# Kernel optimization log

Measured on AMD Instinct MI355X. Metric: run time of the kernel, lower is better.

## Reference

```python
import jax, jax.numpy as jnp
import numpy as np

L, N, H = 32768, 256, 256


def _binop(ei, ej):
    a_i, bu_i = ei
    a_j, bu_j = ej
    return (a_j * a_i, a_j * bu_i + bu_j)


def setup_inputs() -> dict:
    key = jax.random.key(0)
    ks = jax.random.split(key, 9)
    # Param values follow init_lru_parameters statistics for numerical sanity.
    u1 = jax.random.uniform(ks[0], (N,), minval=1e-3, maxval=1.0)
    u2 = jax.random.uniform(ks[1], (N,), minval=1e-3, maxval=1.0)
    nu_log = jnp.log(-0.5 * jnp.log(u1))
    theta_log = jnp.log(6.28 * u2)
    B_re = jax.random.normal(ks[2], (N, H)) / np.sqrt(2.0 * H)
    B_im = jax.random.normal(ks[3], (N, H)) / np.sqrt(2.0 * H)
    C_re = jax.random.normal(ks[4], (H, N)) / np.sqrt(1.0 * N)
    C_im = jax.random.normal(ks[5], (H, N)) / np.sqrt(1.0 * N)
    D = jax.random.normal(ks[6], (H,))
    diag_lambda = jnp.exp(-jnp.exp(nu_log) + 1j * jnp.exp(theta_log))
    gamma_log = jnp.log(jnp.sqrt(1.0 - jnp.abs(diag_lambda) ** 2))
    x = jax.random.normal(ks[7], (L, H), dtype=jnp.float32)
    f32 = lambda a: a.astype(jnp.float32)
    return {"x": x, "nu_log": f32(nu_log), "theta_log": f32(theta_log),
            "B_re": f32(B_re), "B_im": f32(B_im), "C_re": f32(C_re),
            "C_im": f32(C_im), "D": f32(D), "gamma_log": f32(gamma_log)}


def reference(x, nu_log, theta_log, B_re, B_im, C_re, C_im, D, gamma_log):
    # Diagonal complex LRU: x_t = Lambda * x_{t-1} + B_norm u_t ; y_t = Re(C x_t) + D*u_t
    Lambda = jnp.exp(-jnp.exp(nu_log) + 1j * jnp.exp(theta_log))        # (N,) complex
    B_norm = (B_re + 1j * B_im) * jnp.exp(gamma_log)[:, None]           # (N,H)
    C = C_re + 1j * C_im                                                # (H,N)
    Bu = x.astype(B_norm.dtype) @ B_norm.T                              # (L,N) complex
    Lam_el = jnp.broadcast_to(Lambda[None, :], Bu.shape)                # (L,N)
    _, states = jax.lax.associative_scan(_binop, (Lam_el, Bu))          # (L,N) complex
    y = (states @ C.T).real + x * D                                     # (L,H) real
    return y
```

## Files before the change

### kernel.cpp

```cpp
#include <hip/hip_runtime.h>

#define L_SEQ 32768
#define NDIM 256
#define HDIM 256
#define NCAT 512
#define LC 64
#define NCHUNK 512

typedef unsigned short u16;
typedef unsigned int u32;
typedef __bf16 bf16x8 __attribute__((ext_vector_type(8)));
typedef float f32x4 __attribute__((ext_vector_type(4)));
typedef __attribute__((address_space(3))) void lds_void;
typedef const __attribute__((address_space(1))) void gbl_void;

__device__ __forceinline__ u16 f2bf(float f) {
  u32 u = __builtin_bit_cast(u32, f);
  u = u + 0x7fffu + ((u >> 16) & 1u);
  return (u16)(u >> 16);
}
__device__ __forceinline__ float bf2f(u16 v) {
  u32 u = ((u32)v) << 16;
  return __builtin_bit_cast(float, u);
}

__global__ __launch_bounds__(256) void prep_kernel(
    const float* __restrict__ x,
    const float* __restrict__ nu_log, const float* __restrict__ theta_log,
    const float* __restrict__ B_re, const float* __restrict__ B_im,
    const float* __restrict__ C_re, const float* __restrict__ C_im,
    const float* __restrict__ gamma_log,
    u16* __restrict__ x_bf, u16* __restrict__ Bcat, u16* __restrict__ Ccat,
    float2* __restrict__ lam, float2* __restrict__ lam64)
{
  const int blk = blockIdx.x, tid = threadIdx.x;
  if (blk < 2048) {
    const float4* src = (const float4*)x;
#pragma unroll
    for (int j = 0; j < 4; ++j) {
      int i = blk * 1024 + j * 256 + tid;
      int r = i >> 6;
      int col = (i & 63) * 4;
      float4 v = src[i];
      int pcol = col ^ ((r & 7) << 3);
      *(ushort4*)(x_bf + (size_t)r * 256 + pcol) =
          make_ushort4(f2bf(v.x), f2bf(v.y), f2bf(v.z), f2bf(v.w));
    }
  } else if (blk < 2560) {
    int pr = blk - 2048;
    int jj = pr >> 1, p = pr & 1;
    float g = expf(gamma_log[jj]);
    const float* src = (p ? B_im : B_re) + (size_t)jj * HDIM;
    int lc = tid ^ ((pr & 7) << 3);
    Bcat[(size_t)pr * HDIM + tid] = f2bf(src[lc] * g);
  } else if (blk < 2816) {
    int ph = blk - 2560;
    int lr = ph ^ ((ph >> 2) & 1);
#pragma unroll
    for (int half = 0; half < 2; ++half) {
      int pcol = half * 256 + tid;
      int kt = pcol >> 5, w = pcol & 31, pc = w >> 3, e = w & 7;
      int lc2 = kt * 32 + (pc ^ (lr & 3)) * 8 + e;
      int jj = lc2 >> 1, p = lc2 & 1;
      float v = p ? -C_im[(size_t)lr * NDIM + jj] : C_re[(size_t)lr * NDIM + jj];
      Ccat[(size_t)ph * NCAT + pcol] = f2bf(v);
    }
  } else {
    float nu_e = expf(nu_log[tid]);
    float th = expf(theta_log[tid]);
    float r = expf(-nu_e);
    lam[tid] = make_float2(r * cosf(th), r * sinf(th));
    float r64 = expf(-(float)LC * nu_e);
    float ph = (float)LC * th;
    lam64[tid] = make_float2(r64 * cosf(ph), r64 * sinf(ph));
  }
}

__global__ __launch_bounds__(256) void gemm1_kernel(
    const u16* __restrict__ A,
    const u16* __restrict__ Bm,
    u16* __restrict__ Cout,
    int M, int N, int K)
{
  constexpr int BM = 128, BN = 128, BK = 64;
  __shared__ u16 lA[BM * BK];
  __shared__ u16 lB[BN * BK];
  const int tid = threadIdx.x;
  const int lane = tid & 63, wave = tid >> 6;
  const int bn = blockIdx.x, bm = blockIdx.y;
  const int row0 = bm * BM, col0 = bn * BN;
  const int wm = (wave >> 1) * 64, wn = (wave & 1) * 64;
  const int fr = lane & 15, fq = lane >> 4;
  const int swz = (fr & 7) << 4;
  const char* lab = (const char*)lA;
  const char* lbb = (const char*)lB;

  f32x4 acc[4][4] = {};
  const int nkt = K / BK;
  for (int kt = 0; kt < nkt; ++kt) {
    const int k0 = kt * BK;
#pragma unroll
    for (int j = 0; j < 4; ++j) {
      int c = j * 256 + tid;
      int r = c >> 3, b = c & 7;
      const u16* ga = A + (size_t)(row0 + r) * K + (k0 + b * 8);
      const u16* gb = Bm + (size_t)(col0 + r) * K + (k0 + b * 8);
      __builtin_amdgcn_global_load_lds((gbl_void*)ga, (lds_void*)&lA[c * 8], 16, 0, 0);
      __builtin_amdgcn_global_load_lds((gbl_void*)gb, (lds_void*)&lB[c * 8], 16, 0, 0);
    }
    __syncthreads();

#pragma unroll
    for (int h = 0; h < 2; ++h) {
      bf16x8 af[4], bfr[4];
      const int ko = (h * 64 + fq * 16) ^ swz;
#pragma unroll
      for (int i = 0; i < 4; ++i) {
        af[i]  = *(const bf16x8*)(lab + (wm + i * 16 + fr) * 128 + ko);
        bfr[i] = *(const bf16x8*)(lbb + (wn + i * 16 + fr) * 128 + ko);
      }
#pragma unroll
      for (int i = 0; i < 4; ++i)
#pragma unroll
        for (int j = 0; j < 4; ++j)
          acc[i][j] = __builtin_amdgcn_mfma_f32_16x16x32_bf16(af[i], bfr[j], acc[i][j], 0, 0, 0);
    }
    __syncthreads();
  }

  const int fq2 = lane >> 4;
#pragma unroll
  for (int i = 0; i < 4; ++i)
#pragma unroll
    for (int j = 0; j < 4; ++j) {
      int cg = col0 + wn + j * 16 + fr;
#pragma unroll
      for (int r = 0; r < 4; ++r) {
        int rg = row0 + wm + i * 16 + fq2 * 4 + r;
        Cout[(size_t)rg * N + cg] = f2bf(acc[i][j][r]);
      }
    }
}

__global__ __launch_bounds__(256) void scan_carry_kernel(
    const ushort2* __restrict__ Bu2, const float2* __restrict__ lam,
    float2* __restrict__ carry)
{
  const int n = threadIdx.x, b = blockIdx.x;
  const float2 la = lam[n];
  float sre = 0.f, sim = 0.f;
  const ushort2* p = Bu2 + (size_t)b * LC * NDIM + n;
#pragma unroll 8
  for (int j = 0; j < LC; ++j) {
    ushort2 bu = p[(size_t)j * NDIM];
    float bre = bf2f(bu.x), bim = bf2f(bu.y);
    float nre = la.x * sre - la.y * sim + bre;
    float nim = la.x * sim + la.y * sre + bim;
    sre = nre; sim = nim;
  }
  carry[(size_t)b * NDIM + n] = make_float2(sre, sim);
}

__global__ __launch_bounds__(512) void carry_scan_kernel(
    const float2* __restrict__ carry, const float2* __restrict__ lam64,
    float2* __restrict__ corr)
{
  __shared__ float4 e[NCHUNK];
  const int n = blockIdx.x;
  const int b = threadIdx.x;
  float2 a = lam64[n];
  float2 v = carry[(size_t)b * NDIM + n];
  e[b] = make_float4(a.x, a.y, v.x, v.y);
  __syncthreads();
#pragma unroll
  for (int d = 1; d < NCHUNK; d <<= 1) {
    float4 prev;
    if (b >= d) prev = e[b - d];
    __syncthreads();
    if (b >= d) {
      float2 ap = make_float2(prev.x, prev.y), vp = make_float2(prev.z, prev.w);
      float2 na, nv;
      na.x = a.x * ap.x - a.y * ap.y;
      na.y = a.x * ap.y + a.y * ap.x;
      nv.x = a.x * vp.x - a.y * vp.y + v.x;
      nv.y = a.x * vp.y + a.y * vp.x + v.y;
      a = na; v = nv;
      e[b] = make_float4(a.x, a.y, v.x, v.y);
    }
    __syncthreads();
  }
  if (b == 0) corr[n] = make_float2(0.f, 0.f);
  if (b < NCHUNK - 1) corr[(size_t)(b + 1) * NDIM + n] = v;
}

__global__ __launch_bounds__(256, 2) void gemm2_kernel(
    const u16* __restrict__ Bu,
    const u16* __restrict__ Cc,
    const float2* __restrict__ lam,
    const float2* __restrict__ corr,
    const u16* __restrict__ xbf,
    const float* __restrict__ Dv,
    float* __restrict__ out)
{
  constexpr int BM = 64, BK = 32, K = NCAT;
  __shared__ u16 sT[BM * K];
  __shared__ u16 lB1[256 * BK];
  const int tid = threadIdx.x;
  const int lane = tid & 63, wave = tid >> 6;
  const int bm = blockIdx.x;
  const int row0 = bm * BM;
  const int wn = wave * 64;
  const int fr = lane & 15, fq = lane >> 4;
  char* sb = (char*)sT;
  const char* cbB = (const char*)lB1;

#pragma unroll
  for (int j = 0; j < 16; ++j) {
    int q = j * 256 + tid;
    int row = q >> 6, off = q & 63;
    const u16* g = Bu + (size_t)(row0 + row) * NCAT + off * 8;
    __builtin_amdgcn_global_load_lds((gbl_void*)g, (lds_void*)&sT[q * 8], 16, 0, 0);
  }
#pragma unroll
  for (int j = 0; j < 4; ++j) {
    int q = j * 256 + tid;
    int row = q >> 2, c = q & 3;
    const u16* g = Cc + (size_t)row * K + c * 8;
    __builtin_amdgcn_global_load_lds((gbl_void*)g, (lds_void*)&lB1[q * 8], 16, 0, 0);
  }
  float2 la = lam[tid];
  float2 c0 = corr[(size_t)bm * NDIM + tid];
  __syncthreads();

  {
    float sre = c0.x, sim = c0.y;
    ushort2 buf[8], nbuf[8];
    const int lb = tid * 4;
#pragma unroll
    for (int s = 0; s < 8; ++s) buf[s] = *(const ushort2*)(sb + s * 1024 + lb);
#pragma unroll
    for (int b8 = 0; b8 < 8; ++b8) {
      if (b8 < 7) {
#pragma unroll
        for (int s = 0; s < 8; ++s)
          nbuf[s] = *(const ushort2*)(sb + (b8 * 8 + 8 + s) * 1024 + lb);
      }
#pragma unroll
      for (int s = 0; s < 8; ++s) {
        int row = b8 * 8 + s;
        float bre = bf2f(buf[s].x), bim = bf2f(buf[s].y);
        float nre = la.x * sre - la.y * sim + bre;
        float nim = la.x * sim + la.y * sre + bim;
        sre = nre; sim = nim;
        *(ushort2*)(sb + row * 1024 + (lb ^ ((row & 7) << 4))) =
            make_ushort2(f2bf(sre), f2bf(sim));
      }
#pragma unroll
      for (int s = 0; s < 8; ++s) buf[s] = nbuf[s];
    }
  }
  __syncthreads();

  f32x4 acc[4][4] = {};
#pragma unroll 1
  for (int kt = 0; kt < 16; ++kt) {
    bf16x8 af[4], bfr[4];
#pragma unroll
    for (int j = 0; j < 4; ++j) {
      int rowb = wn + j * 16 + fr;
      bfr[j] = *(const bf16x8*)(cbB + ((rowb * 64 + fq * 16) ^ ((rowb & 7) << 4)));
    }
#pragma unroll
    for (int i = 0; i < 4; ++i) {
      int row = i * 16 + fr;
      int wb = kt * 64 + fq * 16;
      af[i] = *(const bf16x8*)(sb + row * 1024 + (wb ^ ((row & 7) << 4)));
    }
    __syncthreads();
    __builtin_amdgcn_sched_barrier(0);
    if (kt < 15) {
#pragma unroll
      for (int j = 0; j < 4; ++j) {
        int q = j * 256 + tid;
        int row = q >> 2, c = q & 3;
        const u16* g = Cc + (size_t)row * K + (kt + 1) * BK + c * 8;
        __builtin_amdgcn_global_load_lds((gbl_void*)g, (lds_void*)&lB1[q * 8], 16, 0, 0);
      }
    }
    __builtin_amdgcn_sched_barrier(0);
#pragma unroll
    for (int i = 0; i < 4; ++i)
#pragma unroll
      for (int j = 0; j < 4; ++j)
        acc[i][j] = __builtin_amdgcn_mfma_f32_16x16x32_bf16(af[i], bfr[j], acc[i][j], 0, 0, 0);
    __syncthreads();
  }

#pragma unroll
  for (int i = 0; i < 4; ++i)
#pragma unroll
    for (int j = 0; j < 4; ++j) {
      int cg = wn + j * 16 + fr;
      float dvc = Dv[cg];
#pragma unroll
      for (int r = 0; r < 4; ++r) {
        int rg = row0 + i * 16 + fq * 4 + r;
        float v = acc[i][j][r] +
                  bf2f(xbf[(size_t)rg * HDIM + (cg ^ ((rg & 7) << 3))]) * dvc;
        out[(size_t)rg * HDIM + cg] = v;
      }
    }
}

extern "C" void kernel_launch(void* const* d_in, const int* in_sizes, int n_in,
                              void* d_out, int out_size, void* d_ws, size_t ws_size,
                              hipStream_t stream)
{
  (void)in_sizes; (void)n_in; (void)out_size; (void)ws_size;
  const float* x         = (const float*)d_in[0];
  const float* nu_log    = (const float*)d_in[1];
  const float* theta_log = (const float*)d_in[2];
  const float* B_re      = (const float*)d_in[3];
  const float* B_im      = (const float*)d_in[4];
  const float* C_re      = (const float*)d_in[5];
  const float* C_im      = (const float*)d_in[6];
  const float* Dv        = (const float*)d_in[7];
  const float* gamma_log = (const float*)d_in[8];

  char* ws = (char*)d_ws;
  u16*    x_bf  = (u16*)ws;
  u16*    Bu_bf = (u16*)(ws + ((size_t)16 << 20));
  u16*    Bcat  = (u16*)(ws + ((size_t)48 << 20));
  u16*    Ccat  = (u16*)(ws + ((size_t)48 << 20) + 262144);
  float2* lam   = (float2*)(ws + ((size_t)48 << 20) + 524288);
  float2* lam64 = (float2*)(ws + ((size_t)48 << 20) + 524288 + 4096);
  float2* carry = (float2*)(ws + ((size_t)49 << 20));
  float2* corr  = (float2*)(ws + ((size_t)50 << 20));

  prep_kernel<<<2817, 256, 0, stream>>>(x, nu_log, theta_log, B_re, B_im,
                                        C_re, C_im, gamma_log,
                                        x_bf, Bcat, Ccat, lam, lam64);

  gemm1_kernel<<<dim3(NCAT / 128, L_SEQ / 128), 256, 0, stream>>>(
      x_bf, Bcat, Bu_bf, L_SEQ, NCAT, HDIM);

  scan_carry_kernel<<<NCHUNK, 256, 0, stream>>>((const ushort2*)Bu_bf, lam, carry);

  carry_scan_kernel<<<NDIM, 512, 0, stream>>>(carry, lam64, corr);

  gemm2_kernel<<<NCHUNK, 256, 0, stream>>>(
      Bu_bf, Ccat, lam, corr, x_bf, Dv, (float*)d_out);
}
```

Measured before the change: 72.51 us.

## Fuse per-chunk carry computation into first GEMM epilogue via lambda-power weighted reduction

Removes the separate scan_carry kernel. Each GEMM1 block now computes each chunk's end-state carry directly from its fp32 accumulators. It weights each row by the matching power of Lambda and reduces across lanes with shuffles. This avoids re-reading the bf16 Bu from memory and a serial 64-step recurrence per chunk, at the cost of extra complex multiplies in the epilogue. The carry now comes from fp32 accumulators rather than bf16-rounded values, which slightly changes the numerics.

```diff
diff --git a/kernel.cpp b/kernel.cpp
--- a/kernel.cpp
+++ b/kernel.cpp
@@ -22,6 +22,9 @@
 __device__ __forceinline__ float bf2f(u16 v) {
   u32 u = ((u32)v) << 16;
   return __builtin_bit_cast(float, u);
+}
+__device__ __forceinline__ float2 cmul(float2 a, float2 b) {
+  return make_float2(a.x * b.x - a.y * b.y, a.x * b.y + a.y * b.x);
 }
 
 __global__ __launch_bounds__(256) void prep_kernel(
@@ -31,7 +34,7 @@
     const float* __restrict__ C_re, const float* __restrict__ C_im,
     const float* __restrict__ gamma_log,
     u16* __restrict__ x_bf, u16* __restrict__ Bcat, u16* __restrict__ Ccat,
-    float2* __restrict__ lam, float2* __restrict__ lam64)
+    float2* __restrict__ lam, float2* __restrict__ lamLC)
 {
   const int blk = blockIdx.x, tid = threadIdx.x;
   if (blk < 2048) {
@@ -70,9 +73,9 @@
     float th = expf(theta_log[tid]);
     float r = expf(-nu_e);
     lam[tid] = make_float2(r * cosf(th), r * sinf(th));
-    float r64 = expf(-(float)LC * nu_e);
+    float rL = expf(-(float)LC * nu_e);
     float ph = (float)LC * th;
-    lam64[tid] = make_float2(r64 * cosf(ph), r64 * sinf(ph));
+    lamLC[tid] = make_float2(rL * cosf(ph), rL * sinf(ph));
   }
 }
 
@@ -80,7 +83,9 @@
     const u16* __restrict__ A,
     const u16* __restrict__ Bm,
     u16* __restrict__ Cout,
-    int M, int N, int K)
+    int M, int N, int K,
+    const float2* __restrict__ lam,
+    float2* __restrict__ carry)
 {
   constexpr int BM = 128, BN = 128, BK = 64;
   __shared__ u16 lA[BM * BK];
@@ -128,7 +133,6 @@
     __syncthreads();
   }
 
-  const int fq2 = lane >> 4;
 #pragma unroll
   for (int i = 0; i < 4; ++i)
 #pragma unroll
@@ -136,39 +140,65 @@
       int cg = col0 + wn + j * 16 + fr;
 #pragma unroll
       for (int r = 0; r < 4; ++r) {
-        int rg = row0 + wm + i * 16 + fq2 * 4 + r;
+        int rg = row0 + wm + i * 16 + fq * 4 + r;
         Cout[(size_t)rg * N + cg] = f2bf(acc[i][j][r]);
       }
     }
-}
-
-__global__ __launch_bounds__(256) void scan_carry_kernel(
-    const ushort2* __restrict__ Bu2, const float2* __restrict__ lam,
-    float2* __restrict__ carry)
-{
-  const int n = threadIdx.x, b = blockIdx.x;
-  const float2 la = lam[n];
-  float sre = 0.f, sim = 0.f;
-  const ushort2* p = Bu2 + (size_t)b * LC * NDIM + n;
-#pragma unroll 8
-  for (int j = 0; j < LC; ++j) {
-    ushort2 bu = p[(size_t)j * NDIM];
-    float bre = bf2f(bu.x), bim = bf2f(bu.y);
-    float nre = la.x * sre - la.y * sim + bre;
-    float nim = la.x * sim + la.y * sre + bim;
-    sre = nre; sim = nim;
-  }
-  carry[(size_t)b * NDIM + n] = make_float2(sre, sim);
+
+  const int chunk = 2 * bm + (wm >> 6);
+#pragma unroll
+  for (int j = 0; j < 4; ++j) {
+    int cg = col0 + wn + j * 16 + fr;
+    float2 L   = lam[cg >> 1];
+    float2 L2  = cmul(L, L);
+    float2 L3  = cmul(L2, L);
+    float2 L4  = cmul(L2, L2);
+    float2 L8  = cmul(L4, L4);
+    float2 L16 = cmul(L8, L8);
+    float2 cBase = (fq == 0) ? cmul(L8, L4)
+                 : (fq == 1) ? L8
+                 : (fq == 2) ? L4
+                 : make_float2(1.f, 0.f);
+    float2 cr[4];
+    cr[3] = cBase;
+    cr[2] = cmul(cBase, L);
+    cr[1] = cmul(cBase, L2);
+    cr[0] = cmul(cBase, L3);
+    float px = 0.f, py = 0.f;
+#pragma unroll
+    for (int i = 3; i >= 0; --i) {
+#pragma unroll
+      for (int r = 0; r < 4; ++r) {
+        float v = acc[i][j][r];
+        px += cr[r].x * v;
+        py += cr[r].y * v;
+      }
+      if (i > 0) {
+#pragma unroll
+        for (int r = 0; r < 4; ++r) cr[r] = cmul(cr[r], L16);
+      }
+    }
+    float cxr = (cg & 1) ? -py : px;
+    float cxi = (cg & 1) ?  px : py;
+    cxr += __shfl_xor(cxr, 1);
+    cxi += __shfl_xor(cxi, 1);
+    cxr += __shfl_xor(cxr, 16);
+    cxi += __shfl_xor(cxi, 16);
+    cxr += __shfl_xor(cxr, 32);
+    cxi += __shfl_xor(cxi, 32);
+    if ((lane & 49) == 0)
+      carry[(size_t)chunk * NDIM + (cg >> 1)] = make_float2(cxr, cxi);
+  }
 }
 
 __global__ __launch_bounds__(512) void carry_scan_kernel(
-    const float2* __restrict__ carry, const float2* __restrict__ lam64,
+    const float2* __restrict__ carry, const float2* __restrict__ lamLC,
     float2* __restrict__ corr)
 {
   __shared__ float4 e[NCHUNK];
   const int n = blockIdx.x;
   const int b = threadIdx.x;
-  float2 a = lam64[n];
+  float2 a = lamLC[n];
   float2 v = carry[(size_t)b * NDIM + n];
   e[b] = make_float4(a.x, a.y, v.x, v.y);
   __syncthreads();
@@ -333,20 +363,18 @@
   u16*    Bcat  = (u16*)(ws + ((size_t)48 << 20));
   u16*    Ccat  = (u16*)(ws + ((size_t)48 << 20) + 262144);
   float2* lam   = (float2*)(ws + ((size_t)48 << 20) + 524288);
-  float2* lam64 = (float2*)(ws + ((size_t)48 << 20) + 524288 + 4096);
+  float2* lamLC = (float2*)(ws + ((size_t)48 << 20) + 524288 + 4096);
   float2* carry = (float2*)(ws + ((size_t)49 << 20));
   float2* corr  = (float2*)(ws + ((size_t)50 << 20));
 
   prep_kernel<<<2817, 256, 0, stream>>>(x, nu_log, theta_log, B_re, B_im,
                                         C_re, C_im, gamma_log,
-                                        x_bf, Bcat, Ccat, lam, lam64);
+                                        x_bf, Bcat, Ccat, lam, lamLC);
 
   gemm1_kernel<<<dim3(NCAT / 128, L_SEQ / 128), 256, 0, stream>>>(
-      x_bf, Bcat, Bu_bf, L_SEQ, NCAT, HDIM);
-
-  scan_carry_kernel<<<NCHUNK, 256, 0, stream>>>((const ushort2*)Bu_bf, lam, carry);
-
-  carry_scan_kernel<<<NDIM, 512, 0, stream>>>(carry, lam64, corr);
+      x_bf, Bcat, Bu_bf, L_SEQ, NCAT, HDIM, lam, carry);
+
+  carry_scan_kernel<<<NDIM, 512, 0, stream>>>(carry, lamLC, corr);
 
   gemm2_kernel<<<NCHUNK, 256, 0, stream>>>(
       Bu_bf, Ccat, lam, corr, x_bf, Dv, (float*)d_out);
```

After: 71.92 us. No clear change (-0.8%).
